# Kernel tuning notes

Hardware: AMD Instinct MI355X
Metric: run time of the kernel (lower is better)

## Reference

```python
import jax, jax.numpy as jnp
import numpy as np

B, N, IN_DIM, D, H, L = 8, 256, 2, 128, 512, 2
EPS = 1e-5


def layer_norm(x, g, b):
    m = jnp.mean(x, axis=-1, keepdims=True)
    v = jnp.var(x, axis=-1, keepdims=True)
    return (x - m) * jax.lax.rsqrt(v + EPS) * g + b


def loo_max_pool(nodes):
    # nodes: (B, N, D) -> leave-one-out max over the set axis -> (B, N, D)
    n = nodes.shape[1]
    neg = jnp.finfo(nodes.dtype).min
    mask = jnp.eye(n, dtype=bool)[None, :, :, None]          # (1, N, N, 1)
    expanded = jnp.broadcast_to(nodes[:, None, :, :],
                                (nodes.shape[0], n, n, nodes.shape[2]))
    return jnp.where(mask, neg, expanded).max(axis=2)        # (B, N, D)


def setup_inputs() -> dict:
    key = jax.random.key(0)
    ks = jax.random.split(key, 16)
    s = 0.02
    inp = {
        "x":   jax.random.normal(ks[0], (B, N, IN_DIM), dtype=jnp.float32),
        # embedding linear + its LayerNorm
        "We":  jax.random.normal(ks[1], (IN_DIM, D)) * s,
        "be":  jnp.zeros((D,), jnp.float32),
        "ge":  jnp.ones((D,), jnp.float32),
        "bge": jnp.zeros((D,), jnp.float32),
        # per-layer pool linear (concat of x and LOO-pooled context: 2D -> D)
        "Wp":  jax.random.normal(ks[2], (L, 2 * D, D)) * s,
        "bp":  jnp.zeros((L, D), jnp.float32),
        "gp":  jnp.ones((L, D), jnp.float32),
        "bgp": jnp.zeros((L, D), jnp.float32),
        # per-layer feed-forward D -> H -> D
        "W1":  jax.random.normal(ks[3], (L, D, H)) * s,
        "b1":  jnp.zeros((L, H), jnp.float32),
        "W2":  jax.random.normal(ks[4], (L, H, D)) * s,
        "b2":  jnp.zeros((L, D), jnp.float32),
        "gf":  jnp.ones((L, D), jnp.float32),
        "bgf": jnp.zeros((L, D), jnp.float32),
    }
    return inp


def reference(x, We, be, ge, bge, Wp, bp, gp, bgp, W1, b1, W2, b2, gf, bgf):
    # embeddings + embedding norm
    h = layer_norm(x @ We + be, ge, bge)                      # (B, N, D)
    for i in range(L):
        # pool layer: LOO max pooling, concat, linear, residual, norm
        pooled = loo_max_pool(h)                              # (B, N, D)
        cat = jnp.concatenate([h, pooled], axis=-1)           # (B, N, 2D)
        h = layer_norm(h + cat @ Wp[i] + bp[i], gp[i], bgp[i])
        # feed-forward, residual, norm
        ff = jax.nn.relu(h @ W1[i] + b1[i]) @ W2[i] + b2[i]
        h = layer_norm(h + ff, gf[i], bgf[i])
    return h
```

## Files before the change

### kernel.cpp

```cpp
#include <hip/hip_runtime.h>
#include <hip/hip_bf16.h>

#define BB 8
#define NN 256
#define DD 128
#define HH 512
#define LL 2
#define EPSV 1e-5f
#define TPB 8
#define BPL (NN/TPB)

typedef unsigned short ushort_t;
typedef __attribute__((ext_vector_type(8))) short bf16x8;
typedef __attribute__((ext_vector_type(4))) float f32x4;

#if defined(__has_builtin)
#if __has_builtin(__builtin_amdgcn_sched_barrier)
#define SCHED_FENCE() __builtin_amdgcn_sched_barrier(0)
#endif
#endif
#ifndef SCHED_FENCE
#define SCHED_FENCE()
#endif

__device__ __forceinline__ ushort_t f2b(float v){
  __hip_bfloat16 h = __float2bfloat16(v);
  return *(ushort_t*)&h;
}

__device__ __forceinline__ void waveRed2(float &a, float &b){
  #pragma unroll
  for (int off=32; off>=1; off>>=1){
    a += __shfl_xor(a, off, 64);
    b += __shfl_xor(b, off, 64);
  }
}

__device__ __forceinline__ void poolMerge(float &m1, float &m2, int &am,
                                          float o1, float o2, int oa){
  if (o1 > m1){ m2 = fmaxf(m1, o2); m1 = o1; am = oa; }
  else        { m2 = fmaxf(m2, o1); }
}

__global__ __launch_bounds__(512, 2) void k_net(
    int layer,
    const float* __restrict__ x, const float* __restrict__ We,
    const float* __restrict__ be, const float* __restrict__ ge,
    const float* __restrict__ bge,
    float* __restrict__ hio,
    float* __restrict__ pm1, float* __restrict__ pm2, int* __restrict__ pma,
    const float* __restrict__ Wp, const float* __restrict__ bp,
    const float* __restrict__ gp, const float* __restrict__ bgp,
    const float* __restrict__ W1, const float* __restrict__ b1,
    const float* __restrict__ W2, const float* __restrict__ b2,
    const float* __restrict__ gf, const float* __restrict__ bgf)
{
  int tid = threadIdx.x;
  int d = tid & 127, fourth = tid >> 7;
  int wv = tid >> 6;
  int lane = tid & 63;
  int m = lane & 15, q = lane >> 4;
  int t0 = blockIdx.x * TPB;
  int b = t0 >> 8;
  int blk = (t0 >> 3) & (BPL-1);

  __shared__ float    hcur[8*128];
  __shared__ ushort_t catb[16*256];
  __shared__ float    sA[16*128];
  __shared__ ushort_t h1b[16*128];
  __shared__ float    h1f[8*128];
  __shared__ ushort_t ub[16*512];
  __shared__ float fm1[128], fm2[128];
  __shared__ int   fam[128];
  __shared__ float sm1[4][128], sm2[4][128];
  __shared__ int   sam[4][128];
  __shared__ float xs[512];
  __shared__ float red9[2][12];
  __shared__ float stats[12];

  if (layer == 0){
    xs[tid] = x[(size_t)b*512 + tid];
    float a = We[d], bw = We[128+d], c = be[d];
    if (fourth == 0){
      float r0=a, r1=bw;        waveRed2(r0,r1);
      float r2=c, r3=a*a;       waveRed2(r2,r3);
      float r4=bw*bw, r5=c*c;   waveRed2(r4,r5);
      float r6=a*bw, r7=a*c;    waveRed2(r6,r7);
      float r8=bw*c, r9=0.f;    waveRed2(r8,r9);
      int w = (tid >> 6) & 1;
      if (lane == 0){
        red9[w][0]=r0; red9[w][1]=r1; red9[w][2]=r2; red9[w][3]=r3;
        red9[w][4]=r4; red9[w][5]=r5; red9[w][6]=r6; red9[w][7]=r7;
        red9[w][8]=r8;
      }
    }
    __syncthreads();
    if (tid < 9) stats[tid] = (red9[0][tid] + red9[1][tid]) * (1.f/128);
    __syncthreads();
    float mA=stats[0], mB=stats[1], mC=stats[2];
    float SAA=stats[3], SBB=stats[4], SCC=stats[5];
    float SAB=stats[6], SAC=stats[7], SBC=stats[8];
    float gev = ge[d], bgev = bge[d];
    float m1=-3.4e38f, m2=-3.4e38f; int am=0;
    for (int i=0;i<64;++i){
      int n = fourth*64 + i;
      float x0 = xs[2*n], x1 = xs[2*n+1];
      float v    = fmaf(x0, a,  fmaf(x1, bw, c));
      float mean = fmaf(x0, mA, fmaf(x1, mB, mC));
      float ev2  = x0*x0*SAA + x1*x1*SBB + SCC
                 + 2.f*(x0*x1*SAB + x0*SAC + x1*SBC);
      float var = ev2 - mean*mean;
      float hv = (v-mean)*rsqrtf(var+EPSV)*gev + bgev;
      poolMerge(m1,m2,am, hv, -3.4e38f, n);
    }
    sm1[fourth][d]=m1; sm2[fourth][d]=m2; sam[fourth][d]=am;
    #pragma unroll
    for (int rep=0; rep<2; ++rep){
      int t = fourth*2 + rep;
      int n = (t0 & 255) + t;
      float x0 = xs[2*n], x1 = xs[2*n+1];
      float v    = fmaf(x0, a,  fmaf(x1, bw, c));
      float mean = fmaf(x0, mA, fmaf(x1, mB, mC));
      float ev2  = x0*x0*SAA + x1*x1*SBB + SCC
                 + 2.f*(x0*x1*SAB + x0*SAC + x1*SBC);
      float var = ev2 - mean*mean;
      hcur[t*128 + d] = (v-mean)*rsqrtf(var+EPSV)*gev + bgev;
    }
    __syncthreads();
  } else {
    {
      size_t base = ((size_t)b*BPL + fourth*8)*128 + d;
      float m1 = pm1[base], m2 = pm2[base]; int am = pma[base];
      #pragma unroll
      for (int i=1;i<8;++i)
        poolMerge(m1,m2,am, pm1[base+(size_t)i*128], pm2[base+(size_t)i*128],
                  pma[base+(size_t)i*128]);
      sm1[fourth][d]=m1; sm2[fourth][d]=m2; sam[fourth][d]=am;
    }
    #pragma unroll
    for (int rep=0; rep<2; ++rep){
      int t = fourth*2 + rep;
      hcur[t*128 + d] = hio[(size_t)(t0+t)*DD + d];
    }
    __syncthreads();
  }

  if (fourth==0){
    float m1=sm1[0][d], m2=sm2[0][d]; int am=sam[0][d];
    #pragma unroll
    for (int p=1;p<4;++p) poolMerge(m1,m2,am, sm1[p][d], sm2[p][d], sam[p][d]);
    fm1[d]=m1; fm2[d]=m2; fam[d]=am;
  }
  __syncthreads();

  #pragma unroll
  for (int rep=0; rep<4; ++rep){
    int e = rep*512 + tid;
    int t = e >> 8, c = e & 255;
    int n = (t0 & 255) + t;
    float v;
    if (c < DD) v = hcur[t*128 + c];
    else { int cc = c - DD; v = (n==fam[cc]) ? fm2[cc] : fm1[cc]; }
    catb[t*256 + c] = f2b(v);
  }
  __syncthreads();

  int n0a = wv*16;

  {
    float wA[8][8];
    #pragma unroll
    for (int ks=0; ks<8; ++ks)
      #pragma unroll
      for (int j=0; j<8; ++j)
        wA[ks][j] = Wp[(size_t)(ks*32 + q*8 + j)*128 + n0a + m];
    SCHED_FENCE();
    f32x4 acc = {0.f,0.f,0.f,0.f};
    const ushort_t* ap = catb + m*256 + q*8;
    #pragma unroll
    for (int ks=0; ks<8; ++ks){
      bf16x8 wf;
      #pragma unroll
      for (int j=0;j<8;++j) wf[j] = (short)f2b(wA[ks][j]);
      bf16x8 af = *(const bf16x8*)(ap + ks*32);
      acc = __builtin_amdgcn_mfma_f32_16x16x32_bf16(af, wf, acc, 0,0,0);
    }
    #pragma unroll
    for (int r=0;r<4;++r) sA[(q*4+r)*128 + n0a + m] = acc[r];
  }
  __syncthreads();

  {
    int t = wv, g = lane;
    float2 v2 = *(const float2*)&sA[t*128 + 2*g];
    float v0 = v2.x + bp[2*g]   + hcur[t*128 + 2*g];
    float v1 = v2.y + bp[2*g+1] + hcur[t*128 + 2*g + 1];
    float s = v0+v1, qq = v0*v0 + v1*v1;
    waveRed2(s,qq);
    float mean = s*(1.f/128), var = qq*(1.f/128) - mean*mean;
    float rs = rsqrtf(var + EPSV);
    float o0 = (v0-mean)*rs*gp[2*g]   + bgp[2*g];
    float o1 = (v1-mean)*rs*gp[2*g+1] + bgp[2*g+1];
    unsigned pk = (unsigned)f2b(o0) | ((unsigned)f2b(o1) << 16);
    *(unsigned*)&h1b[t*128 + 2*g] = pk;
    *(float2*)&h1f[t*128 + 2*g] = make_float2(o0, o1);
  }
  __syncthreads();

  {
    const ushort_t* ap = h1b + m*128 + q*8;
    bf16x8 af[4];
    #pragma unroll
    for (int ks=0; ks<4; ++ks) af[ks] = *(const bf16x8*)(ap + ks*32);
    #pragma unroll
    for (int half=0; half<2; ++half){
      float wB[8][8];
      #pragma unroll
      for (int i=0;i<2;++i){
        int n0 = (half*2+i)*128 + wv*16;
        #pragma unroll
        for (int ks=0; ks<4; ++ks)
          #pragma unroll
          for (int j=0;j<8;++j)
            wB[i*4+ks][j] = W1[(size_t)(ks*32 + q*8 + j)*512 + n0 + m];
      }
      SCHED_FENCE();
      #pragma unroll
      for (int i=0;i<2;++i){
        int n0 = (half*2+i)*128 + wv*16;
        f32x4 acc = {0.f,0.f,0.f,0.f};
        #pragma unroll
        for (int ks=0; ks<4; ++ks){
          bf16x8 wf;
          #pragma unroll
          for (int j=0;j<8;++j) wf[j] = (short)f2b(wB[i*4+ks][j]);
          acc = __builtin_amdgcn_mfma_f32_16x16x32_bf16(af[ks], wf, acc, 0,0,0);
        }
        float bb = b1[n0+m];
        #pragma unroll
        for (int r=0;r<4;++r)
          ub[(q*4+r)*512 + n0 + m] = f2b(fmaxf(acc[r] + bb, 0.f));
      }
    }
  }
  __syncthreads();

  {
    f32x4 acc = {0.f,0.f,0.f,0.f};
    const ushort_t* ap = ub + m*512 + q*8;
    #pragma unroll
    for (int half=0; half<2; ++half){
      float wC[8][8];
      #pragma unroll
      for (int ks=0; ks<8; ++ks)
        #pragma unroll
        for (int j=0;j<8;++j)
          wC[ks][j] = W2[(size_t)((half*8+ks)*32 + q*8 + j)*128 + n0a + m];
      SCHED_FENCE();
      #pragma unroll
      for (int ks=0; ks<8; ++ks){
        bf16x8 wf;
        #pragma unroll
        for (int j=0;j<8;++j) wf[j] = (short)f2b(wC[ks][j]);
        bf16x8 af = *(const bf16x8*)(ap + (half*8+ks)*32);
        acc = __builtin_amdgcn_mfma_f32_16x16x32_bf16(af, wf, acc, 0,0,0);
      }
    }
    #pragma unroll
    for (int r=0;r<4;++r) sA[(q*4+r)*128 + n0a + m] = acc[r];
  }
  __syncthreads();

  {
    int t = wv, g = lane;
    float2 v2 = *(const float2*)&sA[t*128 + 2*g];
    float v0 = v2.x + b2[2*g]   + h1f[t*128 + 2*g];
    float v1 = v2.y + b2[2*g+1] + h1f[t*128 + 2*g + 1];
    float s = v0+v1, qq = v0*v0 + v1*v1;
    waveRed2(s,qq);
    float mean = s*(1.f/128), var = qq*(1.f/128) - mean*mean;
    float rs = rsqrtf(var + EPSV);
    float o0 = (v0-mean)*rs*gf[2*g]   + bgf[2*g];
    float o1 = (v1-mean)*rs*gf[2*g+1] + bgf[2*g+1];
    *(float2*)&hio[(size_t)(t0+t)*DD + 2*g] = make_float2(o0, o1);
    *(float2*)&hcur[t*128 + 2*g] = make_float2(o0, o1);
  }
  if (layer == 0){
    __syncthreads();
    if (tid < 128){
      int n0 = t0 & 255;
      float m1 = hcur[tid], m2 = -3.4e38f; int am = n0;
      #pragma unroll
      for (int p=1;p<TPB;++p)
        poolMerge(m1,m2,am, hcur[p*128+tid], -3.4e38f, n0+p);
      size_t idx = ((size_t)b*BPL + blk)*128 + tid;
      pm1[idx]=m1; pm2[idx]=m2; pma[idx]=am;
    }
  }
}

extern "C" void kernel_launch(void* const* d_in, const int* in_sizes, int n_in,
                              void* d_out, int out_size, void* d_ws, size_t ws_size,
                              hipStream_t stream)
{
  const float* x   = (const float*)d_in[0];
  const float* We  = (const float*)d_in[1];
  const float* be  = (const float*)d_in[2];
  const float* ge  = (const float*)d_in[3];
  const float* bge = (const float*)d_in[4];
  const float* Wp  = (const float*)d_in[5];
  const float* bp  = (const float*)d_in[6];
  const float* gp  = (const float*)d_in[7];
  const float* bgp = (const float*)d_in[8];
  const float* W1  = (const float*)d_in[9];
  const float* b1  = (const float*)d_in[10];
  const float* W2  = (const float*)d_in[11];
  const float* b2  = (const float*)d_in[12];
  const float* gf  = (const float*)d_in[13];
  const float* bgf = (const float*)d_in[14];

  float* hio = (float*)d_out;
  char* ws = (char*)d_ws;
  const size_t NP = (size_t)BB*BPL*128;
  float* p1 = (float*)ws;            ws += NP*4;
  float* p2 = (float*)ws;            ws += NP*4;
  int*   pa = (int*)ws;              ws += NP*4;

  const int grid = (BB*NN)/TPB;

  k_net<<<grid, 512, 0, stream>>>(0, x, We, be, ge, bge, hio, p1, p2, pa,
      Wp,                    bp,      gp,      bgp,
      W1,                    b1,      W2,      b2,
      gf,                    bgf);

  k_net<<<grid, 512, 0, stream>>>(1, x, We, be, ge, bge, hio, p1, p2, pa,
      Wp + (size_t)2*DD*DD,  bp + DD, gp + DD, bgp + DD,
      W1 + (size_t)DD*HH,    b1 + HH, W2 + (size_t)HH*DD, b2 + DD,
      gf + DD,               bgf + DD);
}
```

Before: 115.8 us.

## Split layers into specialized kernels and pre-transpose layer-1 weights to bf16

The single layer-parameterized kernel is split into a layer-0 kernel and a layer-1 kernel. At its tail, the layer-0 kernel uses its first 160 blocks to convert and transpose the layer-1 weight matrices into bf16 buffers in the workspace. The layer-1 kernel then loads its MFMA B-fragments as contiguous 16-byte vectors, instead of doing strided fp32 gathers and bf16 conversion in every block. This adds extra tail work and global writes to the layer-0 kernel and keeps more weight fragments in registers, which may raise register pressure in layer 1.

```diff
diff --git a/kernel.cpp b/kernel.cpp
--- a/kernel.cpp
+++ b/kernel.cpp
@@ -42,8 +42,7 @@
   else        { m2 = fmaxf(m2, o1); }
 }
 
-__global__ __launch_bounds__(512, 2) void k_net(
-    int layer,
+__global__ __launch_bounds__(512, 2) void k_l0(
     const float* __restrict__ x, const float* __restrict__ We,
     const float* __restrict__ be, const float* __restrict__ ge,
     const float* __restrict__ bge,
@@ -53,7 +52,11 @@
     const float* __restrict__ gp, const float* __restrict__ bgp,
     const float* __restrict__ W1, const float* __restrict__ b1,
     const float* __restrict__ W2, const float* __restrict__ b2,
-    const float* __restrict__ gf, const float* __restrict__ bgf)
+    const float* __restrict__ gf, const float* __restrict__ bgf,
+    const float* __restrict__ Wp1, const float* __restrict__ W11,
+    const float* __restrict__ W21,
+    ushort_t* __restrict__ wpT, ushort_t* __restrict__ w1T,
+    ushort_t* __restrict__ w2T)
 {
   int tid = threadIdx.x;
   int d = tid & 127, fourth = tid >> 7;
@@ -78,25 +81,25 @@
   __shared__ float red9[2][12];
   __shared__ float stats[12];
 
-  if (layer == 0){
-    xs[tid] = x[(size_t)b*512 + tid];
-    float a = We[d], bw = We[128+d], c = be[d];
-    if (fourth == 0){
-      float r0=a, r1=bw;        waveRed2(r0,r1);
-      float r2=c, r3=a*a;       waveRed2(r2,r3);
-      float r4=bw*bw, r5=c*c;   waveRed2(r4,r5);
-      float r6=a*bw, r7=a*c;    waveRed2(r6,r7);
-      float r8=bw*c, r9=0.f;    waveRed2(r8,r9);
-      int w = (tid >> 6) & 1;
-      if (lane == 0){
-        red9[w][0]=r0; red9[w][1]=r1; red9[w][2]=r2; red9[w][3]=r3;
-        red9[w][4]=r4; red9[w][5]=r5; red9[w][6]=r6; red9[w][7]=r7;
-        red9[w][8]=r8;
-      }
-    }
-    __syncthreads();
-    if (tid < 9) stats[tid] = (red9[0][tid] + red9[1][tid]) * (1.f/128);
-    __syncthreads();
+  xs[tid] = x[(size_t)b*512 + tid];
+  float a = We[d], bw = We[128+d], c = be[d];
+  if (fourth == 0){
+    float r0=a, r1=bw;        waveRed2(r0,r1);
+    float r2=c, r3=a*a;       waveRed2(r2,r3);
+    float r4=bw*bw, r5=c*c;   waveRed2(r4,r5);
+    float r6=a*bw, r7=a*c;    waveRed2(r6,r7);
+    float r8=bw*c, r9=0.f;    waveRed2(r8,r9);
+    int w = (tid >> 6) & 1;
+    if (lane == 0){
+      red9[w][0]=r0; red9[w][1]=r1; red9[w][2]=r2; red9[w][3]=r3;
+      red9[w][4]=r4; red9[w][5]=r5; red9[w][6]=r6; red9[w][7]=r7;
+      red9[w][8]=r8;
+    }
+  }
+  __syncthreads();
+  if (tid < 9) stats[tid] = (red9[0][tid] + red9[1][tid]) * (1.f/128);
+  __syncthreads();
+  {
     float mA=stats[0], mB=stats[1], mC=stats[2];
     float SAA=stats[3], SBB=stats[4], SCC=stats[5];
     float SAB=stats[6], SAC=stats[7], SBC=stats[8];
@@ -126,25 +129,8 @@
       float var = ev2 - mean*mean;
       hcur[t*128 + d] = (v-mean)*rsqrtf(var+EPSV)*gev + bgev;
     }
-    __syncthreads();
-  } else {
-    {
-      size_t base = ((size_t)b*BPL + fourth*8)*128 + d;
-      float m1 = pm1[base], m2 = pm2[base]; int am = pma[base];
-      #pragma unroll
-      for (int i=1;i<8;++i)
-        poolMerge(m1,m2,am, pm1[base+(size_t)i*128], pm2[base+(size_t)i*128],
-                  pma[base+(size_t)i*128]);
-      sm1[fourth][d]=m1; sm2[fourth][d]=m2; sam[fourth][d]=am;
-    }
-    #pragma unroll
-    for (int rep=0; rep<2; ++rep){
-      int t = fourth*2 + rep;
-      hcur[t*128 + d] = hio[(size_t)(t0+t)*DD + d];
-    }
-    __syncthreads();
-  }
-
+  }
+  __syncthreads();
   if (fourth==0){
     float m1=sm1[0][d], m2=sm2[0][d]; int am=sam[0][d];
     #pragma unroll
@@ -156,12 +142,12 @@
   #pragma unroll
   for (int rep=0; rep<4; ++rep){
     int e = rep*512 + tid;
-    int t = e >> 8, c = e & 255;
+    int t = e >> 8, cc = e & 255;
     int n = (t0 & 255) + t;
     float v;
-    if (c < DD) v = hcur[t*128 + c];
-    else { int cc = c - DD; v = (n==fam[cc]) ? fm2[cc] : fm1[cc]; }
-    catb[t*256 + c] = f2b(v);
+    if (cc < DD) v = hcur[t*128 + cc];
+    else { int c2 = cc - DD; v = (n==fam[c2]) ? fm2[c2] : fm1[c2]; }
+    catb[t*256 + cc] = f2b(v);
   }
   __syncthreads();
 
@@ -285,17 +271,197 @@
     *(float2*)&hio[(size_t)(t0+t)*DD + 2*g] = make_float2(o0, o1);
     *(float2*)&hcur[t*128 + 2*g] = make_float2(o0, o1);
   }
-  if (layer == 0){
-    __syncthreads();
-    if (tid < 128){
-      int n0 = t0 & 255;
-      float m1 = hcur[tid], m2 = -3.4e38f; int am = n0;
-      #pragma unroll
-      for (int p=1;p<TPB;++p)
-        poolMerge(m1,m2,am, hcur[p*128+tid], -3.4e38f, n0+p);
-      size_t idx = ((size_t)b*BPL + blk)*128 + tid;
-      pm1[idx]=m1; pm2[idx]=m2; pma[idx]=am;
-    }
+  __syncthreads();
+  if (tid < 128){
+    int n0 = t0 & 255;
+    float m1 = hcur[tid], m2 = -3.4e38f; int am = n0;
+    #pragma unroll
+    for (int p=1;p<TPB;++p)
+      poolMerge(m1,m2,am, hcur[p*128+tid], -3.4e38f, n0+p);
+    size_t idx = ((size_t)b*BPL + blk)*128 + tid;
+    pm1[idx]=m1; pm2[idx]=m2; pma[idx]=am;
+  }
+
+  if (blockIdx.x < 160 && tid < 256){
+    int bid = blockIdx.x;
+    const float* src; ushort_t* dst; int K, N, kt, nt;
+    if (bid < 32){ src = Wp1; dst = wpT; K=256; N=128; kt = bid>>2; nt = bid&3; }
+    else if (bid < 96){ int e=bid-32; src = W11; dst = w1T; K=128; N=512; kt = e>>4; nt = e&15; }
+    else { int e=bid-96; src = W21; dst = w2T; K=512; N=128; kt = e>>2; nt = e&3; }
+    int k0 = kt*32, n0 = nt*32;
+    int tx = tid & 31, ty = (tid >> 5) & 7;
+    #pragma unroll
+    for (int i=0;i<4;++i)
+      dst[(size_t)(n0+ty+i*8)*K + k0 + tx] =
+        f2b(src[(size_t)(k0+tx)*N + n0 + ty + i*8]);
+  }
+}
+
+__global__ __launch_bounds__(512, 2) void k_l1(
+    float* __restrict__ hio,
+    const float* __restrict__ pm1, const float* __restrict__ pm2,
+    const int* __restrict__ pma,
+    const ushort_t* __restrict__ wpT, const float* __restrict__ bp,
+    const float* __restrict__ gp, const float* __restrict__ bgp,
+    const ushort_t* __restrict__ w1T, const float* __restrict__ b1,
+    const ushort_t* __restrict__ w2T, const float* __restrict__ b2,
+    const float* __restrict__ gf, const float* __restrict__ bgf)
+{
+  int tid = threadIdx.x;
+  int d = tid & 127, fourth = tid >> 7;
+  int wv = tid >> 6;
+  int lane = tid & 63;
+  int m = lane & 15, q = lane >> 4;
+  int t0 = blockIdx.x * TPB;
+  int b = t0 >> 8;
+
+  __shared__ float    hcur[8*128];
+  __shared__ ushort_t catb[16*256];
+  __shared__ float    sA[16*128];
+  __shared__ ushort_t h1b[16*128];
+  __shared__ float    h1f[8*128];
+  __shared__ ushort_t ub[16*512];
+  __shared__ float fm1[128], fm2[128];
+  __shared__ int   fam[128];
+  __shared__ float sm1[4][128], sm2[4][128];
+  __shared__ int   sam[4][128];
+
+  int n0a = wv*16;
+
+  bf16x8 wfA[8];
+  {
+    const ushort_t* wp = wpT + (size_t)(n0a+m)*256 + q*8;
+    #pragma unroll
+    for (int ks=0; ks<8; ++ks) wfA[ks] = *(const bf16x8*)(wp + ks*32);
+  }
+  bf16x8 wfB[16];
+  {
+    #pragma unroll
+    for (int i=0;i<4;++i){
+      int n0 = i*128 + wv*16;
+      const ushort_t* wp = w1T + (size_t)(n0+m)*128 + q*8;
+      #pragma unroll
+      for (int ks=0; ks<4; ++ks) wfB[i*4+ks] = *(const bf16x8*)(wp + ks*32);
+    }
+  }
+  bf16x8 wfC[16];
+  {
+    const ushort_t* wp = w2T + (size_t)(n0a+m)*512 + q*8;
+    #pragma unroll
+    for (int ks=0; ks<16; ++ks) wfC[ks] = *(const bf16x8*)(wp + ks*32);
+  }
+  SCHED_FENCE();
+
+  {
+    size_t base = ((size_t)b*BPL + fourth*8)*128 + d;
+    float m1 = pm1[base], m2 = pm2[base]; int am = pma[base];
+    #pragma unroll
+    for (int i=1;i<8;++i)
+      poolMerge(m1,m2,am, pm1[base+(size_t)i*128], pm2[base+(size_t)i*128],
+                pma[base+(size_t)i*128]);
+    sm1[fourth][d]=m1; sm2[fourth][d]=m2; sam[fourth][d]=am;
+  }
+  #pragma unroll
+  for (int rep=0; rep<2; ++rep){
+    int t = fourth*2 + rep;
+    hcur[t*128 + d] = hio[(size_t)(t0+t)*DD + d];
+  }
+  __syncthreads();
+  if (fourth==0){
+    float m1=sm1[0][d], m2=sm2[0][d]; int am=sam[0][d];
+    #pragma unroll
+    for (int p=1;p<4;++p) poolMerge(m1,m2,am, sm1[p][d], sm2[p][d], sam[p][d]);
+    fm1[d]=m1; fm2[d]=m2; fam[d]=am;
+  }
+  __syncthreads();
+
+  #pragma unroll
+  for (int rep=0; rep<4; ++rep){
+    int e = rep*512 + tid;
+    int t = e >> 8, cc = e & 255;
+    int n = (t0 & 255) + t;
+    float v;
+    if (cc < DD) v = hcur[t*128 + cc];
+    else { int c2 = cc - DD; v = (n==fam[c2]) ? fm2[c2] : fm1[c2]; }
+    catb[t*256 + cc] = f2b(v);
+  }
+  __syncthreads();
+
+  {
+    f32x4 acc = {0.f,0.f,0.f,0.f};
+    const ushort_t* ap = catb + m*256 + q*8;
+    #pragma unroll
+    for (int ks=0; ks<8; ++ks){
+      bf16x8 af = *(const bf16x8*)(ap + ks*32);
+      acc = __builtin_amdgcn_mfma_f32_16x16x32_bf16(af, wfA[ks], acc, 0,0,0);
+    }
+    #pragma unroll
+    for (int r=0;r<4;++r) sA[(q*4+r)*128 + n0a + m] = acc[r];
+  }
+  __syncthreads();
+
+  {
+    int t = wv, g = lane;
+    float2 v2 = *(const float2*)&sA[t*128 + 2*g];
+    float v0 = v2.x + bp[2*g]   + hcur[t*128 + 2*g];
+    float v1 = v2.y + bp[2*g+1] + hcur[t*128 + 2*g + 1];
+    float s = v0+v1, qq = v0*v0 + v1*v1;
+    waveRed2(s,qq);
+    float mean = s*(1.f/128), var = qq*(1.f/128) - mean*mean;
+    float rs = rsqrtf(var + EPSV);
+    float o0 = (v0-mean)*rs*gp[2*g]   + bgp[2*g];
+    float o1 = (v1-mean)*rs*gp[2*g+1] + bgp[2*g+1];
+    unsigned pk = (unsigned)f2b(o0) | ((unsigned)f2b(o1) << 16);
+    *(unsigned*)&h1b[t*128 + 2*g] = pk;
+    *(float2*)&h1f[t*128 + 2*g] = make_float2(o0, o1);
+  }
+  __syncthreads();
+
+  {
+    const ushort_t* ap = h1b + m*128 + q*8;
+    bf16x8 af[4];
+    #pragma unroll
+    for (int ks=0; ks<4; ++ks) af[ks] = *(const bf16x8*)(ap + ks*32);
+    #pragma unroll
+    for (int i=0;i<4;++i){
+      int n0 = i*128 + wv*16;
+      f32x4 acc = {0.f,0.f,0.f,0.f};
+      #pragma unroll
+      for (int ks=0; ks<4; ++ks)
+        acc = __builtin_amdgcn_mfma_f32_16x16x32_bf16(af[ks], wfB[i*4+ks], acc, 0,0,0);
+      float bb = b1[n0+m];
+      #pragma unroll
+      for (int r=0;r<4;++r)
+        ub[(q*4+r)*512 + n0 + m] = f2b(fmaxf(acc[r] + bb, 0.f));
+    }
+  }
+  __syncthreads();
+
+  {
+    f32x4 acc = {0.f,0.f,0.f,0.f};
+    const ushort_t* ap = ub + m*512 + q*8;
+    #pragma unroll
+    for (int ks=0; ks<16; ++ks){
+      bf16x8 af = *(const bf16x8*)(ap + ks*32);
+      acc = __builtin_amdgcn_mfma_f32_16x16x32_bf16(af, wfC[ks], acc, 0,0,0);
+    }
+    #pragma unroll
+    for (int r=0;r<4;++r) sA[(q*4+r)*128 + n0a + m] = acc[r];
+  }
+  __syncthreads();
+
+  {
+    int t = wv, g = lane;
+    float2 v2 = *(const float2*)&sA[t*128 + 2*g];
+    float v0 = v2.x + b2[2*g]   + h1f[t*128 + 2*g];
+    float v1 = v2.y + b2[2*g+1] + h1f[t*128 + 2*g + 1];
+    float s = v0+v1, qq = v0*v0 + v1*v1;
+    waveRed2(s,qq);
+    float mean = s*(1.f/128), var = qq*(1.f/128) - mean*mean;
+    float rs = rsqrtf(var + EPSV);
+    float o0 = (v0-mean)*rs*gf[2*g]   + bgf[2*g];
+    float o1 = (v1-mean)*rs*gf[2*g+1] + bgf[2*g+1];
+    *(float2*)&hio[(size_t)(t0+t)*DD + 2*g] = make_float2(o0, o1);
   }
 }
 
@@ -325,16 +491,21 @@
   float* p1 = (float*)ws;            ws += NP*4;
   float* p2 = (float*)ws;            ws += NP*4;
   int*   pa = (int*)ws;              ws += NP*4;
+  ushort_t* wpT = (ushort_t*)ws;     ws += (size_t)128*256*2;
+  ushort_t* w1T = (ushort_t*)ws;     ws += (size_t)512*128*2;
+  ushort_t* w2T = (ushort_t*)ws;     ws += (size_t)128*512*2;
 
   const int grid = (BB*NN)/TPB;
 
-  k_net<<<grid, 512, 0, stream>>>(0, x, We, be, ge, bge, hio, p1, p2, pa,
+  k_l0<<<grid, 512, 0, stream>>>(x, We, be, ge, bge, hio, p1, p2, pa,
       Wp,                    bp,      gp,      bgp,
       W1,                    b1,      W2,      b2,
-      gf,                    bgf);
-
-  k_net<<<grid, 512, 0, stream>>>(1, x, We, be, ge, bge, hio, p1, p2, pa,
-      Wp + (size_t)2*DD*DD,  bp + DD, gp + DD, bgp + DD,
-      W1 + (size_t)DD*HH,    b1 + HH, W2 + (size_t)HH*DD, b2 + DD,
-      gf + DD,               bgf + DD);
+      gf,                    bgf,
+      Wp + (size_t)2*DD*DD,  W1 + (size_t)DD*HH,  W2 + (size_t)HH*DD,
+      wpT, w1T, w2T);
+
+  k_l1<<<grid, 512, 0, stream>>>(hio, p1, p2, pa,
+      wpT, bp + DD, gp + DD, bgp + DD,
+      w1T, b1 + HH, w2T, b2 + DD,
+      gf + DD, bgf + DD);
 }
```

Result: slower. 118.4 us (+2.2%).

## Fuse both layers into one kernel by recomputing layer 0 per block

Applied to the files above, without the earlier changes.

Merges the two per-layer launches into one kernel. Each block recomputes layer 0 for its whole set in 16-row tiles, collecting the leave-one-out max statistics locally instead of exchanging them through a global workspace. Layer-0 Wp and W1 weights are preloaded into registers as bf16 fragments and reused across tiles. This removes a launch and the global pooling round-trip, but multiplies layer-0 compute per block by roughly the number of blocks per batch and raises register pressure.

```diff
diff --git a/kernel.cpp b/kernel.cpp
--- a/kernel.cpp
+++ b/kernel.cpp
@@ -5,10 +5,7 @@
 #define NN 256
 #define DD 128
 #define HH 512
-#define LL 2
 #define EPSV 1e-5f
-#define TPB 8
-#define BPL (NN/TPB)
 
 typedef unsigned short ushort_t;
 typedef __attribute__((ext_vector_type(8))) short bf16x8;
@@ -42,44 +39,68 @@
   else        { m2 = fmaxf(m2, o1); }
 }
 
-__global__ __launch_bounds__(512, 2) void k_net(
-    int layer,
+__global__ __launch_bounds__(512, 2) void k_all(
     const float* __restrict__ x, const float* __restrict__ We,
     const float* __restrict__ be, const float* __restrict__ ge,
     const float* __restrict__ bge,
-    float* __restrict__ hio,
-    float* __restrict__ pm1, float* __restrict__ pm2, int* __restrict__ pma,
-    const float* __restrict__ Wp, const float* __restrict__ bp,
-    const float* __restrict__ gp, const float* __restrict__ bgp,
-    const float* __restrict__ W1, const float* __restrict__ b1,
-    const float* __restrict__ W2, const float* __restrict__ b2,
-    const float* __restrict__ gf, const float* __restrict__ bgf)
+    const float* __restrict__ Wp0, const float* __restrict__ bp0,
+    const float* __restrict__ gp0, const float* __restrict__ bgp0,
+    const float* __restrict__ W10, const float* __restrict__ b10,
+    const float* __restrict__ W20, const float* __restrict__ b20,
+    const float* __restrict__ gf0, const float* __restrict__ bgf0,
+    const float* __restrict__ Wp1, const float* __restrict__ bp1,
+    const float* __restrict__ gp1, const float* __restrict__ bgp1,
+    const float* __restrict__ W11, const float* __restrict__ b11,
+    const float* __restrict__ W21, const float* __restrict__ b21,
+    const float* __restrict__ gf1, const float* __restrict__ bgf1,
+    float* __restrict__ hio)
 {
   int tid = threadIdx.x;
   int d = tid & 127, fourth = tid >> 7;
   int wv = tid >> 6;
   int lane = tid & 63;
   int m = lane & 15, q = lane >> 4;
-  int t0 = blockIdx.x * TPB;
-  int b = t0 >> 8;
-  int blk = (t0 >> 3) & (BPL-1);
-
-  __shared__ float    hcur[8*128];
+  int t0 = blockIdx.x * 8;
+  int b = blockIdx.x >> 5;
+  int nown = t0 & 255;
+
+  __shared__ float    xs[512];
+  __shared__ float    red9[2][12];
+  __shared__ float    stats[12];
+  __shared__ float    hres[16*128];
   __shared__ ushort_t catb[16*256];
   __shared__ float    sA[16*128];
   __shared__ ushort_t h1b[16*128];
-  __shared__ float    h1f[8*128];
+  __shared__ float    h1f[16*128];
   __shared__ ushort_t ub[16*512];
+  __shared__ float    hown[8*128];
   __shared__ float fm1[128], fm2[128];
   __shared__ int   fam[128];
   __shared__ float sm1[4][128], sm2[4][128];
   __shared__ int   sam[4][128];
-  __shared__ float xs[512];
-  __shared__ float red9[2][12];
-  __shared__ float stats[12];
-
-  if (layer == 0){
-    xs[tid] = x[(size_t)b*512 + tid];
+
+  int n0a = wv*16;
+
+  float wAf[8][8];
+  #pragma unroll
+  for (int ks=0; ks<8; ++ks)
+    #pragma unroll
+    for (int j=0; j<8; ++j)
+      wAf[ks][j] = Wp0[(size_t)(ks*32 + q*8 + j)*128 + n0a + m];
+  float wBf[16][8];
+  #pragma unroll
+  for (int i=0;i<4;++i){
+    int n0 = i*128 + wv*16;
+    #pragma unroll
+    for (int ks=0; ks<4; ++ks)
+      #pragma unroll
+      for (int j=0;j<8;++j)
+        wBf[i*4+ks][j] = W10[(size_t)(ks*32 + q*8 + j)*512 + n0 + m];
+  }
+  SCHED_FENCE();
+
+  xs[tid] = x[(size_t)b*512 + tid];
+  {
     float a = We[d], bw = We[128+d], c = be[d];
     if (fourth == 0){
       float r0=a, r1=bw;        waveRed2(r0,r1);
@@ -114,58 +135,178 @@
       poolMerge(m1,m2,am, hv, -3.4e38f, n);
     }
     sm1[fourth][d]=m1; sm2[fourth][d]=m2; sam[fourth][d]=am;
-    #pragma unroll
-    for (int rep=0; rep<2; ++rep){
-      int t = fourth*2 + rep;
-      int n = (t0 & 255) + t;
-      float x0 = xs[2*n], x1 = xs[2*n+1];
-      float v    = fmaf(x0, a,  fmaf(x1, bw, c));
-      float mean = fmaf(x0, mA, fmaf(x1, mB, mC));
-      float ev2  = x0*x0*SAA + x1*x1*SBB + SCC
-                 + 2.f*(x0*x1*SAB + x0*SAC + x1*SBC);
-      float var = ev2 - mean*mean;
-      hcur[t*128 + d] = (v-mean)*rsqrtf(var+EPSV)*gev + bgev;
-    }
-    __syncthreads();
-  } else {
-    {
-      size_t base = ((size_t)b*BPL + fourth*8)*128 + d;
-      float m1 = pm1[base], m2 = pm2[base]; int am = pma[base];
-      #pragma unroll
-      for (int i=1;i<8;++i)
-        poolMerge(m1,m2,am, pm1[base+(size_t)i*128], pm2[base+(size_t)i*128],
-                  pma[base+(size_t)i*128]);
-      sm1[fourth][d]=m1; sm2[fourth][d]=m2; sam[fourth][d]=am;
-    }
-    #pragma unroll
-    for (int rep=0; rep<2; ++rep){
-      int t = fourth*2 + rep;
-      hcur[t*128 + d] = hio[(size_t)(t0+t)*DD + d];
-    }
-    __syncthreads();
-  }
-
+  }
+  __syncthreads();
   if (fourth==0){
     float m1=sm1[0][d], m2=sm2[0][d]; int am=sam[0][d];
     #pragma unroll
     for (int p=1;p<4;++p) poolMerge(m1,m2,am, sm1[p][d], sm2[p][d], sam[p][d]);
     fm1[d]=m1; fm2[d]=m2; fam[d]=am;
   }
+  SCHED_FENCE();
+  bf16x8 wfA[8];
+  #pragma unroll
+  for (int ks=0; ks<8; ++ks)
+    #pragma unroll
+    for (int j=0;j<8;++j) wfA[ks][j] = (short)f2b(wAf[ks][j]);
+  bf16x8 wfB[16];
+  #pragma unroll
+  for (int kk=0; kk<16; ++kk)
+    #pragma unroll
+    for (int j=0;j<8;++j) wfB[kk][j] = (short)f2b(wBf[kk][j]);
+  __syncthreads();
+
+  float r_m1 = -3.4e38f, r_m2 = -3.4e38f; int r_am = 0;
+  float mA=stats[0], mB=stats[1], mC=stats[2];
+  float SAA=stats[3], SBB=stats[4], SCC=stats[5];
+  float SAB=stats[6], SAC=stats[7], SBC=stats[8];
+
+  for (int tile=0; tile<16; ++tile){
+    int nbase = tile*16;
+    {
+      float gev = ge[d], bgev = bge[d];
+      #pragma unroll
+      for (int rep=0; rep<4; ++rep){
+        int t = rep*4 + fourth;
+        int n = nbase + t;
+        float x0 = xs[2*n], x1 = xs[2*n+1];
+        float v    = fmaf(x0, We[d],  fmaf(x1, We[128+d], be[d]));
+        float mean = fmaf(x0, mA, fmaf(x1, mB, mC));
+        float ev2  = x0*x0*SAA + x1*x1*SBB + SCC
+                   + 2.f*(x0*x1*SAB + x0*SAC + x1*SBC);
+        float var = ev2 - mean*mean;
+        float hv = (v-mean)*rsqrtf(var+EPSV)*gev + bgev;
+        hres[t*128 + d] = hv;
+        catb[t*256 + d] = f2b(hv);
+        float pv = (n == fam[d]) ? fm2[d] : fm1[d];
+        catb[t*256 + 128 + d] = f2b(pv);
+      }
+    }
+    __syncthreads();
+
+    {
+      f32x4 acc = {0.f,0.f,0.f,0.f};
+      const ushort_t* ap = catb + m*256 + q*8;
+      #pragma unroll
+      for (int ks=0; ks<8; ++ks){
+        bf16x8 af = *(const bf16x8*)(ap + ks*32);
+        acc = __builtin_amdgcn_mfma_f32_16x16x32_bf16(af, wfA[ks], acc, 0,0,0);
+      }
+      #pragma unroll
+      for (int r=0;r<4;++r) sA[(q*4+r)*128 + n0a + m] = acc[r];
+    }
+    __syncthreads();
+
+    #pragma unroll
+    for (int half=0; half<2; ++half){
+      int t = wv + half*8, g = lane;
+      float2 v2 = *(const float2*)&sA[t*128 + 2*g];
+      float v0 = v2.x + bp0[2*g]   + hres[t*128 + 2*g];
+      float v1 = v2.y + bp0[2*g+1] + hres[t*128 + 2*g + 1];
+      float s = v0+v1, qq = v0*v0 + v1*v1;
+      waveRed2(s,qq);
+      float mean = s*(1.f/128), var = qq*(1.f/128) - mean*mean;
+      float rs = rsqrtf(var + EPSV);
+      float o0 = (v0-mean)*rs*gp0[2*g]   + bgp0[2*g];
+      float o1 = (v1-mean)*rs*gp0[2*g+1] + bgp0[2*g+1];
+      unsigned pk = (unsigned)f2b(o0) | ((unsigned)f2b(o1) << 16);
+      *(unsigned*)&h1b[t*128 + 2*g] = pk;
+      *(float2*)&h1f[t*128 + 2*g] = make_float2(o0, o1);
+    }
+    __syncthreads();
+
+    {
+      const ushort_t* ap = h1b + m*128 + q*8;
+      bf16x8 af[4];
+      #pragma unroll
+      for (int ks=0; ks<4; ++ks) af[ks] = *(const bf16x8*)(ap + ks*32);
+      #pragma unroll
+      for (int i=0;i<4;++i){
+        int n0 = i*128 + wv*16;
+        f32x4 acc = {0.f,0.f,0.f,0.f};
+        #pragma unroll
+        for (int ks=0; ks<4; ++ks)
+          acc = __builtin_amdgcn_mfma_f32_16x16x32_bf16(af[ks], wfB[i*4+ks], acc, 0,0,0);
+        float bb = b10[n0+m];
+        #pragma unroll
+        for (int r=0;r<4;++r)
+          ub[(q*4+r)*512 + n0 + m] = f2b(fmaxf(acc[r] + bb, 0.f));
+      }
+    }
+    __syncthreads();
+
+    {
+      f32x4 acc = {0.f,0.f,0.f,0.f};
+      const ushort_t* ap = ub + m*512 + q*8;
+      #pragma unroll
+      for (int half=0; half<2; ++half){
+        float wC[8][8];
+        #pragma unroll
+        for (int ks=0; ks<8; ++ks)
+          #pragma unroll
+          for (int j=0;j<8;++j)
+            wC[ks][j] = W20[(size_t)((half*8+ks)*32 + q*8 + j)*128 + n0a + m];
+        SCHED_FENCE();
+        #pragma unroll
+        for (int ks=0; ks<8; ++ks){
+          bf16x8 wf;
+          #pragma unroll
+          for (int j=0;j<8;++j) wf[j] = (short)f2b(wC[ks][j]);
+          bf16x8 af = *(const bf16x8*)(ap + (half*8+ks)*32);
+          acc = __builtin_amdgcn_mfma_f32_16x16x32_bf16(af, wf, acc, 0,0,0);
+        }
+      }
+      #pragma unroll
+      for (int r=0;r<4;++r) sA[(q*4+r)*128 + n0a + m] = acc[r];
+    }
+    __syncthreads();
+
+    #pragma unroll
+    for (int half=0; half<2; ++half){
+      int t = wv + half*8, g = lane;
+      float2 v2 = *(const float2*)&sA[t*128 + 2*g];
+      float v0 = v2.x + b20[2*g]   + h1f[t*128 + 2*g];
+      float v1 = v2.y + b20[2*g+1] + h1f[t*128 + 2*g + 1];
+      float s = v0+v1, qq = v0*v0 + v1*v1;
+      waveRed2(s,qq);
+      float mean = s*(1.f/128), var = qq*(1.f/128) - mean*mean;
+      float rs = rsqrtf(var + EPSV);
+      float o0 = (v0-mean)*rs*gf0[2*g]   + bgf0[2*g];
+      float o1 = (v1-mean)*rs*gf0[2*g+1] + bgf0[2*g+1];
+      *(float2*)&hres[t*128 + 2*g] = make_float2(o0, o1);
+    }
+    __syncthreads();
+
+    if (tid < 128){
+      #pragma unroll
+      for (int p=0;p<16;++p)
+        poolMerge(r_m1, r_m2, r_am, hres[p*128 + tid], -3.4e38f, nbase + p);
+    }
+    if (tile == (nown >> 4)){
+      int r0 = nown & 15;
+      #pragma unroll
+      for (int rep=0; rep<2; ++rep){
+        int t = fourth*2 + rep;
+        hown[t*128 + d] = hres[(r0 + t)*128 + d];
+      }
+    }
+    __syncthreads();
+  }
+
+  if (tid < 128){ fm1[tid] = r_m1; fm2[tid] = r_m2; fam[tid] = r_am; }
   __syncthreads();
 
   #pragma unroll
   for (int rep=0; rep<4; ++rep){
     int e = rep*512 + tid;
-    int t = e >> 8, c = e & 255;
-    int n = (t0 & 255) + t;
+    int t = e >> 8, cc = e & 255;
+    int n = nown + t;
     float v;
-    if (c < DD) v = hcur[t*128 + c];
-    else { int cc = c - DD; v = (n==fam[cc]) ? fm2[cc] : fm1[cc]; }
-    catb[t*256 + c] = f2b(v);
-  }
-  __syncthreads();
-
-  int n0a = wv*16;
+    if (cc < DD) v = hown[t*128 + cc];
+    else { int c2 = cc - DD; v = (n==fam[c2]) ? fm2[c2] : fm1[c2]; }
+    catb[t*256 + cc] = f2b(v);
+  }
+  __syncthreads();
 
   {
     float wA[8][8];
@@ -173,7 +314,7 @@
     for (int ks=0; ks<8; ++ks)
       #pragma unroll
       for (int j=0; j<8; ++j)
-        wA[ks][j] = Wp[(size_t)(ks*32 + q*8 + j)*128 + n0a + m];
+        wA[ks][j] = Wp1[(size_t)(ks*32 + q*8 + j)*128 + n0a + m];
     SCHED_FENCE();
     f32x4 acc = {0.f,0.f,0.f,0.f};
     const ushort_t* ap = catb + m*256 + q*8;
@@ -193,14 +334,14 @@
   {
     int t = wv, g = lane;
     float2 v2 = *(const float2*)&sA[t*128 + 2*g];
-    float v0 = v2.x + bp[2*g]   + hcur[t*128 + 2*g];
-    float v1 = v2.y + bp[2*g+1] + hcur[t*128 + 2*g + 1];
+    float v0 = v2.x + bp1[2*g]   + hown[t*128 + 2*g];
+    float v1 = v2.y + bp1[2*g+1] + hown[t*128 + 2*g + 1];
     float s = v0+v1, qq = v0*v0 + v1*v1;
     waveRed2(s,qq);
     float mean = s*(1.f/128), var = qq*(1.f/128) - mean*mean;
     float rs = rsqrtf(var + EPSV);
-    float o0 = (v0-mean)*rs*gp[2*g]   + bgp[2*g];
-    float o1 = (v1-mean)*rs*gp[2*g+1] + bgp[2*g+1];
+    float o0 = (v0-mean)*rs*gp1[2*g]   + bgp1[2*g];
+    float o1 = (v1-mean)*rs*gp1[2*g+1] + bgp1[2*g+1];
     unsigned pk = (unsigned)f2b(o0) | ((unsigned)f2b(o1) << 16);
     *(unsigned*)&h1b[t*128 + 2*g] = pk;
     *(float2*)&h1f[t*128 + 2*g] = make_float2(o0, o1);
@@ -222,7 +363,7 @@
         for (int ks=0; ks<4; ++ks)
           #pragma unroll
           for (int j=0;j<8;++j)
-            wB[i*4+ks][j] = W1[(size_t)(ks*32 + q*8 + j)*512 + n0 + m];
+            wB[i*4+ks][j] = W11[(size_t)(ks*32 + q*8 + j)*512 + n0 + m];
       }
       SCHED_FENCE();
       #pragma unroll
@@ -236,7 +377,7 @@
           for (int j=0;j<8;++j) wf[j] = (short)f2b(wB[i*4+ks][j]);
           acc = __builtin_amdgcn_mfma_f32_16x16x32_bf16(af[ks], wf, acc, 0,0,0);
         }
-        float bb = b1[n0+m];
+        float bb = b11[n0+m];
         #pragma unroll
         for (int r=0;r<4;++r)
           ub[(q*4+r)*512 + n0 + m] = f2b(fmaxf(acc[r] + bb, 0.f));
@@ -255,7 +396,7 @@
       for (int ks=0; ks<8; ++ks)
         #pragma unroll
         for (int j=0;j<8;++j)
-          wC[ks][j] = W2[(size_t)((half*8+ks)*32 + q*8 + j)*128 + n0a + m];
+          wC[ks][j] = W21[(size_t)((half*8+ks)*32 + q*8 + j)*128 + n0a + m];
       SCHED_FENCE();
       #pragma unroll
       for (int ks=0; ks<8; ++ks){
@@ -274,28 +415,15 @@
   {
     int t = wv, g = lane;
     float2 v2 = *(const float2*)&sA[t*128 + 2*g];
-    float v0 = v2.x + b2[2*g]   + h1f[t*128 + 2*g];
-    float v1 = v2.y + b2[2*g+1] + h1f[t*128 + 2*g + 1];
+    float v0 = v2.x + b21[2*g]   + h1f[t*128 + 2*g];
+    float v1 = v2.y + b21[2*g+1] + h1f[t*128 + 2*g + 1];
     float s = v0+v1, qq = v0*v0 + v1*v1;
     waveRed2(s,qq);
     float mean = s*(1.f/128), var = qq*(1.f/128) - mean*mean;
     float rs = rsqrtf(var + EPSV);
-    float o0 = (v0-mean)*rs*gf[2*g]   + bgf[2*g];
-    float o1 = (v1-mean)*rs*gf[2*g+1] + bgf[2*g+1];
+    float o0 = (v0-mean)*rs*gf1[2*g]   + bgf1[2*g];
+    float o1 = (v1-mean)*rs*gf1[2*g+1] + bgf1[2*g+1];
     *(float2*)&hio[(size_t)(t0+t)*DD + 2*g] = make_float2(o0, o1);
-    *(float2*)&hcur[t*128 + 2*g] = make_float2(o0, o1);
-  }
-  if (layer == 0){
-    __syncthreads();
-    if (tid < 128){
-      int n0 = t0 & 255;
-      float m1 = hcur[tid], m2 = -3.4e38f; int am = n0;
-      #pragma unroll
-      for (int p=1;p<TPB;++p)
-        poolMerge(m1,m2,am, hcur[p*128+tid], -3.4e38f, n0+p);
-      size_t idx = ((size_t)b*BPL + blk)*128 + tid;
-      pm1[idx]=m1; pm2[idx]=m2; pma[idx]=am;
-    }
   }
 }
 
@@ -318,23 +446,14 @@
   const float* b2  = (const float*)d_in[12];
   const float* gf  = (const float*)d_in[13];
   const float* bgf = (const float*)d_in[14];
-
   float* hio = (float*)d_out;
-  char* ws = (char*)d_ws;
-  const size_t NP = (size_t)BB*BPL*128;
-  float* p1 = (float*)ws;            ws += NP*4;
-  float* p2 = (float*)ws;            ws += NP*4;
-  int*   pa = (int*)ws;              ws += NP*4;
-
-  const int grid = (BB*NN)/TPB;
-
-  k_net<<<grid, 512, 0, stream>>>(0, x, We, be, ge, bge, hio, p1, p2, pa,
-      Wp,                    bp,      gp,      bgp,
-      W1,                    b1,      W2,      b2,
-      gf,                    bgf);
-
-  k_net<<<grid, 512, 0, stream>>>(1, x, We, be, ge, bge, hio, p1, p2, pa,
-      Wp + (size_t)2*DD*DD,  bp + DD, gp + DD, bgp + DD,
-      W1 + (size_t)DD*HH,    b1 + HH, W2 + (size_t)HH*DD, b2 + DD,
-      gf + DD,               bgf + DD);
+
+  k_all<<<(BB*NN)/8, 512, 0, stream>>>(x, We, be, ge, bge,
+      Wp,                    bp,       gp,       bgp,
+      W1,                    b1,       W2,       b2,
+      gf,                    bgf,
+      Wp + (size_t)2*DD*DD,  bp + DD,  gp + DD,  bgp + DD,
+      W1 + (size_t)DD*HH,    b1 + HH,  W2 + (size_t)HH*DD, b2 + DD,
+      gf + DD,               bgf + DD,
+      hio);
 }
```

New measurement: 351.8 us. +203.8%, slower.
